# Kernel optimization log

Hardware: AMD Instinct MI355X
Metric: run time of the kernel (lower is better)

Reference implementation:

```python
import jax, jax.numpy as jnp
import numpy as np


def setup_inputs() -> dict:
    key = jax.random.key(0)
    ks = jax.random.split(key, 8)
    B = 65536
    x = jax.random.normal(ks[0], (B, 784), dtype=jnp.float32)
    conv_w = jnp.ones((3, 3), dtype=jnp.float32)  # Parameter(ones((3,3)))
    # Linear layers stored as (in, out) weight + (out,) bias
    def lin(k, fin, fout):
        kw, kb = jax.random.split(k)
        bound = 1.0 / np.sqrt(fin)
        W = jax.random.uniform(kw, (fin, fout), minval=-bound, maxval=bound, dtype=jnp.float32)
        b = jax.random.uniform(kb, (fout,), minval=-bound, maxval=bound, dtype=jnp.float32)
        return W, b
    W1, b1 = lin(ks[1], 26 * 26, 500)
    W2, b2 = lin(ks[2], 500, 200)
    W3, b3 = lin(ks[3], 200, 10)
    return {"x": x, "conv_w": conv_w, "W1": W1, "b1": b1,
            "W2": W2, "b2": b2, "W3": W3, "b3": b3}


def reference(x, conv_w, W1, b1, W2, b2, W3, b3):
    B = x.shape[0]
    img = x.reshape(B, 1, 28, 28)  # NCHW, single channel
    kern = conv_w.reshape(1, 1, 3, 3)  # OIHW
    # valid 2D cross-correlation == torch tensordot sliding-window loop
    conv = jax.lax.conv_general_dilated(
        img, kern, window_strides=(1, 1), padding='VALID',
        dimension_numbers=('NCHW', 'OIHW', 'NCHW'))  # (B,1,26,26)
    h = conv.reshape(B, 26 * 26)
    h = jax.nn.relu(h @ W1 + b1)
    h = jax.nn.relu(h @ W2 + b2)
    return h @ W3 + b3  # (B, 10) logits
```

## Files before the change

kernel.cpp:

```cpp
#include <hip/hip_runtime.h>
#include <hip/hip_bf16.h>
#include <stdint.h>

typedef __bf16 bf16x8 __attribute__((ext_vector_type(8)));
typedef float  f32x4  __attribute__((ext_vector_type(4)));


#define KT1 25
#define NF1 32
#define KT2 16
#define NF2 16
#define KT3 8

__global__ void prep_w1(const float* __restrict__ W1, const float* __restrict__ cw,
                        __bf16* __restrict__ w1s) {
  int gid  = blockIdx.x * 256 + threadIdx.x;
  int lane = gid & 63;
  int slot = gid >> 6;
  int t = slot >> 5;
  int f = slot & 31;
  int kbase = t * 32 + ((lane >> 4) << 3);
  int n = f * 16 + (lane & 15);
  float c[9];
#pragma unroll
  for (int i = 0; i < 9; ++i) c[i] = cw[i];
  bf16x8 v;
#pragma unroll
  for (int e = 0; e < 8; ++e) {
    int k = kbase + e;
    float acc = 0.f;
    if (k < 784 && n < 500) {
      int pi = k / 28, pj = k % 28;
#pragma unroll
      for (int dr = 0; dr < 3; ++dr) {
        int r = pi - dr;
        if (r < 0 || r >= 26) continue;
#pragma unroll
        for (int dc = 0; dc < 3; ++dc) {
          int cc = pj - dc;
          if (cc < 0 || cc >= 26) continue;
          acc += c[dr * 3 + dc] * W1[(size_t)(r * 26 + cc) * 500 + n];
        }
      }
    }
    v[e] = (__bf16)acc;
  }
  *(bf16x8*)(w1s + (size_t)(slot * 64 + lane) * 8) = v;
}

__global__ void prep_w2(const float* __restrict__ W2, __bf16* __restrict__ w2s) {
  int gid  = blockIdx.x * 256 + threadIdx.x;
  int lane = gid & 63;
  int slot = gid >> 6;
  int t = slot >> 4;
  int f = slot & 15;
  int kbase = t * 32 + ((lane >> 4) << 3);
  int n = f * 16 + (lane & 15);
  bf16x8 v;
#pragma unroll
  for (int e = 0; e < 8; ++e) {
    int k = kbase + e;
    float val = (k < 500 && n < 200) ? W2[(size_t)k * 200 + n] : 0.f;
    v[e] = (__bf16)val;
  }
  *(bf16x8*)(w2s + (size_t)(slot * 64 + lane) * 8) = v;
}

__global__ void prep_w3(const float* __restrict__ W3, __bf16* __restrict__ w3s) {
  int gid  = blockIdx.x * 256 + threadIdx.x;
  int lane = gid & 63;
  int t    = gid >> 6;
  int kbase = t * 32 + ((lane >> 4) << 3);
  int n = lane & 15;
  bf16x8 v;
#pragma unroll
  for (int e = 0; e < 8; ++e) {
    int k = kbase + e;
    float val = (k < 200 && n < 10) ? W3[(size_t)k * 10 + n] : 0.f;
    v[e] = (__bf16)val;
  }
  *(bf16x8*)(w3s + (size_t)(t * 64 + lane) * 8) = v;
}

__global__ __launch_bounds__(256, 2) void mlp_fused(
    const float* __restrict__ x,
    const __bf16* __restrict__ w1s, const __bf16* __restrict__ w2s,
    const __bf16* __restrict__ w3s,
    const float* __restrict__ b1, const float* __restrict__ b2,
    const float* __restrict__ b3,
    float* __restrict__ out)
{
  __shared__ __align__(16) char smem[64 * 1024];
  __shared__ float sb1[512];
  __shared__ float sb2[256];

  const int tid  = threadIdx.x;
  const int lane = tid & 63;
  const int w    = tid >> 6;
  const int lrow = lane & 15;
  const int lgrp = lane >> 4;
  const int brow = blockIdx.x * 64;
  const int xr   = tid >> 2;
  const int xq   = tid & 3;

  sb1[tid]       = (tid < 500) ? b1[tid] : 0.f;
  sb1[tid + 256] = (tid + 256 < 500) ? b1[tid + 256] : 0.f;
  sb2[tid]       = (tid < 200) ? b2[tid] : 0.f;

  const f32x4 FZ = {0.f, 0.f, 0.f, 0.f};

  f32x4 acc1[4][8];
#pragma unroll
  for (int m = 0; m < 4; ++m)
#pragma unroll
    for (int f = 0; f < 8; ++f) acc1[m][f] = FZ;

  const bf16x8* w1p   = (const bf16x8*)w1s + ((size_t)(w * 8) * 64 + lane);
  const float*  xbase = x + (size_t)(brow + xr) * 784;
  const int     xoff  = xr * 64 + ((xq ^ (xr & 3)) << 4);

  f32x4 g[4][2];

  auto gload4 = [&](int s) {
#pragma unroll
    for (int j = 0; j < 4; ++j) {
      int tile = s * 4 + j;
      if (tile > 24) tile = 24;
      int gk = tile * 32 + xq * 8;
      if (gk > 776) gk = 776;
      const float* p = xbase + gk;
      g[j][0] = *(const f32x4*)p;
      g[j][1] = *(const f32x4*)(p + 4);
    }
  };
  auto cwrite4 = [&](int buf) {
#pragma unroll
    for (int j = 0; j < 4; ++j) {
      bf16x8 v;
#pragma unroll
      for (int e = 0; e < 4; ++e) { v[e] = (__bf16)g[j][0][e]; v[e + 4] = (__bf16)g[j][1][e]; }
      *(bf16x8*)(smem + buf * 16384 + j * 4096 + xoff) = v;
    }
  };

  bf16x8 bA[8], bB[8];

  auto ktile = [&](int tile, int rb, int slot, bf16x8 (&bc)[8], bf16x8 (&bn)[8], bool pf) {
    bf16x8 afr[4];
#pragma unroll
    for (int m = 0; m < 4; ++m) {
      int r = m * 16 + lrow;
      afr[m] = *(const bf16x8*)(smem + rb + slot * 4096 + r * 64 + ((lgrp ^ (r & 3)) << 4));
    }
    if (pf) {
#pragma unroll
      for (int f = 0; f < 8; ++f) bn[f] = w1p[(size_t)((tile + 1) * NF1 + f) * 64];
    }
    __builtin_amdgcn_s_setprio(1);
#pragma unroll
    for (int f = 0; f < 8; ++f)
#pragma unroll
      for (int m = 0; m < 4; ++m)
        acc1[m][f] = __builtin_amdgcn_mfma_f32_16x16x32_bf16(afr[m], bc[f], acc1[m][f], 0, 0, 0);
    __builtin_amdgcn_s_setprio(0);
  };

  gload4(0);
#pragma unroll
  for (int f = 0; f < 8; ++f) bA[f] = w1p[(size_t)f * 64];
  cwrite4(0);
  asm volatile("s_waitcnt lgkmcnt(0)\n\ts_barrier" ::: "memory");

  for (int s = 0; s < 6; ++s) {
    int rb = (s & 1) * 16384;
    gload4(s + 1);
    int t0 = s * 4;
    ktile(t0 + 0, rb, 0, bA, bB, true);
    ktile(t0 + 1, rb, 1, bB, bA, true);
    ktile(t0 + 2, rb, 2, bA, bB, true);
    ktile(t0 + 3, rb, 3, bB, bA, true);
    cwrite4((s + 1) & 1);
    asm volatile("s_waitcnt lgkmcnt(0)\n\ts_barrier" ::: "memory");
  }
  ktile(24, 0, 0, bA, bB, false);

  const bf16x8* w2p = (const bf16x8*)w2s + ((size_t)(w * 4) * 64 + lane);
  bf16x8 b2a[4], b2b[4];
#pragma unroll
  for (int f = 0; f < 4; ++f) b2a[f] = w2p[(size_t)f * 64];

  asm volatile("s_waitcnt lgkmcnt(0)\n\ts_barrier" ::: "memory");

#pragma unroll
  for (int m = 0; m < 4; ++m) {
#pragma unroll
    for (int f = 0; f < 8; ++f) {
      int col = w * 128 + f * 16 + lrow;
      float bias = sb1[col];
#pragma unroll
      for (int r = 0; r < 4; ++r) {
        int row = m * 16 + lgrp * 4 + r;
        float v = fmaxf(acc1[m][f][r] + bias, 0.f);
        int off = row * 1024 + ((col * 2) ^ ((row & 7) << 4));
        *(__bf16*)(smem + off) = (__bf16)v;
      }
    }
  }
  __syncthreads();

  f32x4 acc2[4][4];
#pragma unroll
  for (int m = 0; m < 4; ++m)
#pragma unroll
    for (int f = 0; f < 4; ++f) acc2[m][f] = FZ;

  for (int t = 0; t < KT2; t += 2) {
#pragma unroll
    for (int f = 0; f < 4; ++f) b2b[f] = w2p[(size_t)((t + 1) * NF2 + f) * 64];
    {
      bf16x8 a2[4];
#pragma unroll
      for (int m = 0; m < 4; ++m) {
        int row = m * 16 + lrow;
        int off = row * 1024 + ((t * 64 + lgrp * 16) ^ ((row & 7) << 4));
        a2[m] = *(const bf16x8*)(smem + off);
      }
      __builtin_amdgcn_s_setprio(1);
#pragma unroll
      for (int f = 0; f < 4; ++f)
#pragma unroll
        for (int m = 0; m < 4; ++m)
          acc2[m][f] = __builtin_amdgcn_mfma_f32_16x16x32_bf16(a2[m], b2a[f], acc2[m][f], 0, 0, 0);
      __builtin_amdgcn_s_setprio(0);
    }
#pragma unroll
    for (int f = 0; f < 4; ++f) b2a[f] = w2p[(size_t)((t + 2) * NF2 + f) * 64];
    {
      bf16x8 a2[4];
#pragma unroll
      for (int m = 0; m < 4; ++m) {
        int row = m * 16 + lrow;
        int off = row * 1024 + (((t + 1) * 64 + lgrp * 16) ^ ((row & 7) << 4));
        a2[m] = *(const bf16x8*)(smem + off);
      }
      __builtin_amdgcn_s_setprio(1);
#pragma unroll
      for (int f = 0; f < 4; ++f)
#pragma unroll
        for (int m = 0; m < 4; ++m)
          acc2[m][f] = __builtin_amdgcn_mfma_f32_16x16x32_bf16(a2[m], b2b[f], acc2[m][f], 0, 0, 0);
      __builtin_amdgcn_s_setprio(0);
    }
  }

  __syncthreads();

#pragma unroll
  for (int m = 0; m < 4; ++m) {
#pragma unroll
    for (int f = 0; f < 4; ++f) {
      int col = w * 64 + f * 16 + lrow;
      float bias = sb2[col];
#pragma unroll
      for (int r = 0; r < 4; ++r) {
        int row = m * 16 + lgrp * 4 + r;
        float v = fmaxf(acc2[m][f][r] + bias, 0.f);
        int off = row * 512 + ((col * 2) ^ ((row & 7) << 4));
        *(__bf16*)(smem + off) = (__bf16)v;
      }
    }
  }
  __syncthreads();

  {
    f32x4 a3 = FZ;
    const bf16x8* w3p = (const bf16x8*)w3s + lane;
#pragma unroll
    for (int t = 0; t < KT3; ++t) {
      int row = w * 16 + lrow;
      int off = row * 512 + ((t * 64 + lgrp * 16) ^ ((row & 7) << 4));
      bf16x8 a = *(const bf16x8*)(smem + off);
      a3 = __builtin_amdgcn_mfma_f32_16x16x32_bf16(a, w3p[(size_t)t * 64], a3, 0, 0, 0);
    }
    if (lrow < 10) {
      float bias = b3[lrow];
#pragma unroll
      for (int r = 0; r < 4; ++r)
        out[(size_t)(brow + w * 16 + lgrp * 4 + r) * 10 + lrow] = a3[r] + bias;
    }
  }
}

extern "C" void kernel_launch(void* const* d_in, const int* in_sizes, int n_in,
                              void* d_out, int out_size, void* d_ws, size_t ws_size,
                              hipStream_t stream) {
  const float* x  = (const float*)d_in[0];
  const float* cw = (const float*)d_in[1];
  const float* W1 = (const float*)d_in[2];
  const float* b1 = (const float*)d_in[3];
  const float* W2 = (const float*)d_in[4];
  const float* b2 = (const float*)d_in[5];
  const float* W3 = (const float*)d_in[6];
  const float* b3 = (const float*)d_in[7];
  float* out = (float*)d_out;

  __bf16* w1s = (__bf16*)d_ws;
  __bf16* w2s = w1s + (size_t)KT1 * NF1 * 64 * 8;
  __bf16* w3s = w2s + (size_t)KT2 * NF2 * 64 * 8;

  prep_w1<<<200, 256, 0, stream>>>(W1, cw, w1s);
  prep_w2<<<64, 256, 0, stream>>>(W2, w2s);
  prep_w3<<<2, 256, 0, stream>>>(W3, w3s);

  mlp_fused<<<65536 / 64, 256, 0, stream>>>(x, w1s, w2s, w3s, b1, b2, b3, out);
}
```

Measured before the change: 99.66 us.

## Use 128-row blocks of 512 threads with W1 tiles staged through LDS

Doubles the block tile to 128 rows with eight waves in a 2x4 grid, so each W1 tile is loaded once per block into LDS via global_load_lds and shared by both row groups, instead of each wave reading B fragments from global memory. The x staging switches from four-tile chunks to per-tile double buffering, with a vmcnt wait overlapping loads of tile t+1 with compute on tile t. LDS grows to 128KB and occupancy drops to one block per CU, which adds a barrier every k-tile and gives less latency hiding. The layer-3 section was not updated for 128 rows in the visible portion, so correctness depends on the hidden code.

```diff
diff --git a/kernel.cpp b/kernel.cpp
--- a/kernel.cpp
+++ b/kernel.cpp
@@ -82,7 +82,12 @@
   *(bf16x8*)(w3s + (size_t)(t * 64 + lane) * 8) = v;
 }
 
-__global__ __launch_bounds__(256, 2) void mlp_fused(
+#define BS0 0
+#define BS1 32768
+#define XS0 65536
+#define XS1 73728
+
+__global__ __launch_bounds__(512, 1) void mlp_fused(
     const float* __restrict__ x,
     const __bf16* __restrict__ w1s, const __bf16* __restrict__ w2s,
     const __bf16* __restrict__ w3s,
@@ -90,22 +95,23 @@
     const float* __restrict__ b3,
     float* __restrict__ out)
 {
-  __shared__ __align__(16) char smem[64 * 1024];
+  __shared__ __align__(16) char smem[128 * 1024];
   __shared__ float sb1[512];
   __shared__ float sb2[256];
 
   const int tid  = threadIdx.x;
   const int lane = tid & 63;
   const int w    = tid >> 6;
+  const int mg   = w >> 2;
+  const int ng   = w & 3;
   const int lrow = lane & 15;
   const int lgrp = lane >> 4;
-  const int brow = blockIdx.x * 64;
+  const int brow = blockIdx.x * 128;
   const int xr   = tid >> 2;
   const int xq   = tid & 3;
 
-  sb1[tid]       = (tid < 500) ? b1[tid] : 0.f;
-  sb1[tid + 256] = (tid + 256 < 500) ? b1[tid + 256] : 0.f;
-  sb2[tid]       = (tid < 200) ? b2[tid] : 0.f;
+  sb1[tid & 511] = ((tid & 511) < 500) ? b1[tid & 511] : 0.f;
+  if (tid < 256) sb2[tid] = (tid < 200) ? b2[tid] : 0.f;
 
   const f32x4 FZ = {0.f, 0.f, 0.f, 0.f};
 
@@ -115,91 +121,87 @@
 #pragma unroll
     for (int f = 0; f < 8; ++f) acc1[m][f] = FZ;
 
-  const bf16x8* w1p   = (const bf16x8*)w1s + ((size_t)(w * 8) * 64 + lane);
-  const float*  xbase = x + (size_t)(brow + xr) * 784;
-  const int     xoff  = xr * 64 + ((xq ^ (xr & 3)) << 4);
-
-  f32x4 g[4][2];
-
-  auto gload4 = [&](int s) {
-#pragma unroll
-    for (int j = 0; j < 4; ++j) {
-      int tile = s * 4 + j;
-      if (tile > 24) tile = 24;
-      int gk = tile * 32 + xq * 8;
-      if (gk > 776) gk = 776;
-      const float* p = xbase + gk;
-      g[j][0] = *(const f32x4*)p;
-      g[j][1] = *(const f32x4*)(p + 4);
-    }
-  };
-  auto cwrite4 = [&](int buf) {
-#pragma unroll
-    for (int j = 0; j < 4; ++j) {
-      bf16x8 v;
-#pragma unroll
-      for (int e = 0; e < 4; ++e) { v[e] = (__bf16)g[j][0][e]; v[e + 4] = (__bf16)g[j][1][e]; }
-      *(bf16x8*)(smem + buf * 16384 + j * 4096 + xoff) = v;
-    }
-  };
-
-  bf16x8 bA[8], bB[8];
-
-  auto ktile = [&](int tile, int rb, int slot, bf16x8 (&bc)[8], bf16x8 (&bn)[8], bool pf) {
-    bf16x8 afr[4];
+  const float* xbase = x + (size_t)(brow + xr) * 784;
+  const int    xwoff = xr * 64 + ((xq ^ (xr & 3)) << 4);
+
+  f32x4 g[2];
+
+  auto xload = [&](int t) {
+    int gk = t * 32 + xq * 8;
+    if (gk > 776) gk = 776;
+    g[0] = *(const f32x4*)(xbase + gk);
+    g[1] = *(const f32x4*)(xbase + gk + 4);
+  };
+  auto xwrite = [&](int buf) {
+    bf16x8 v;
+#pragma unroll
+    for (int e = 0; e < 4; ++e) { v[e] = (__bf16)g[0][e]; v[e + 4] = (__bf16)g[1][e]; }
+    *(bf16x8*)(smem + buf + xwoff) = v;
+  };
+  auto stage_b = [&](int tile, int buf) {
+    const char* src = (const char*)w1s + (size_t)tile * 32768 + w * 4096 + lane * 16;
+#pragma unroll
+    for (int i = 0; i < 4; ++i)
+      __builtin_amdgcn_global_load_lds(
+          (const __attribute__((address_space(1))) void*)(src + i * 1024),
+          (__attribute__((address_space(3))) void*)(smem + buf + w * 4096 + i * 1024),
+          16, 0, 0);
+  };
+  auto ktile = [&](int xbuf, int bbuf) {
+    bf16x8 afr[4], bfr[8];
 #pragma unroll
     for (int m = 0; m < 4; ++m) {
-      int r = m * 16 + lrow;
-      afr[m] = *(const bf16x8*)(smem + rb + slot * 4096 + r * 64 + ((lgrp ^ (r & 3)) << 4));
-    }
-    if (pf) {
-#pragma unroll
-      for (int f = 0; f < 8; ++f) bn[f] = w1p[(size_t)((tile + 1) * NF1 + f) * 64];
-    }
+      int r = mg * 64 + m * 16 + lrow;
+      afr[m] = *(const bf16x8*)(smem + xbuf + r * 64 + ((lgrp ^ (r & 3)) << 4));
+    }
+#pragma unroll
+    for (int f = 0; f < 8; ++f)
+      bfr[f] = *(const bf16x8*)(smem + bbuf + (ng * 8 + f) * 1024 + lane * 16);
     __builtin_amdgcn_s_setprio(1);
 #pragma unroll
     for (int f = 0; f < 8; ++f)
 #pragma unroll
       for (int m = 0; m < 4; ++m)
-        acc1[m][f] = __builtin_amdgcn_mfma_f32_16x16x32_bf16(afr[m], bc[f], acc1[m][f], 0, 0, 0);
+        acc1[m][f] = __builtin_amdgcn_mfma_f32_16x16x32_bf16(afr[m], bfr[f], acc1[m][f], 0, 0, 0);
     __builtin_amdgcn_s_setprio(0);
   };
-
-  gload4(0);
-#pragma unroll
-  for (int f = 0; f < 8; ++f) bA[f] = w1p[(size_t)f * 64];
-  cwrite4(0);
-  asm volatile("s_waitcnt lgkmcnt(0)\n\ts_barrier" ::: "memory");
-
-  for (int s = 0; s < 6; ++s) {
-    int rb = (s & 1) * 16384;
-    gload4(s + 1);
-    int t0 = s * 4;
-    ktile(t0 + 0, rb, 0, bA, bB, true);
-    ktile(t0 + 1, rb, 1, bB, bA, true);
-    ktile(t0 + 2, rb, 2, bA, bB, true);
-    ktile(t0 + 3, rb, 3, bB, bA, true);
-    cwrite4((s + 1) & 1);
+  auto body = [&](int t, int xcur, int bcur, int xnxt, int bnxt) {
+    xload(t + 1);
+    stage_b(t + 1, bnxt);
+    asm volatile("s_waitcnt vmcnt(6)" ::: "memory");
+    ktile(xcur, bcur);
+    xwrite(xnxt);
     asm volatile("s_waitcnt lgkmcnt(0)\n\ts_barrier" ::: "memory");
-  }
-  ktile(24, 0, 0, bA, bB, false);
-
-  const bf16x8* w2p = (const bf16x8*)w2s + ((size_t)(w * 4) * 64 + lane);
+  };
+
+  xload(0);
+  stage_b(0, BS0);
+  xwrite(0 + XS0);
+  asm volatile("s_waitcnt vmcnt(0) lgkmcnt(0)\n\ts_barrier" ::: "memory");
+
+  for (int t = 0; t < 24; t += 2) {
+    body(t,     XS0, BS0, XS1, BS1);
+    body(t + 1, XS1, BS1, XS0, BS0);
+  }
+  asm volatile("s_waitcnt vmcnt(0)" ::: "memory");
+  ktile(XS0, BS0);
+
+  const bf16x8* w2p = (const bf16x8*)w2s + ((size_t)(ng * 4) * 64 + lane);
   bf16x8 b2a[4], b2b[4];
 #pragma unroll
   for (int f = 0; f < 4; ++f) b2a[f] = w2p[(size_t)f * 64];
 
-  asm volatile("s_waitcnt lgkmcnt(0)\n\ts_barrier" ::: "memory");
+  __syncthreads();
 
 #pragma unroll
   for (int m = 0; m < 4; ++m) {
 #pragma unroll
     for (int f = 0; f < 8; ++f) {
-      int col = w * 128 + f * 16 + lrow;
+      int col = ng * 128 + f * 16 + lrow;
       float bias = sb1[col];
 #pragma unroll
       for (int r = 0; r < 4; ++r) {
-        int row = m * 16 + lgrp * 4 + r;
+        int row = mg * 64 + m * 16 + lgrp * 4 + r;
         float v = fmaxf(acc1[m][f][r] + bias, 0.f);
         int off = row * 1024 + ((col * 2) ^ ((row & 7) << 4));
         *(__bf16*)(smem + off) = (__bf16)v;
@@ -221,7 +223,7 @@
       bf16x8 a2[4];
 #pragma unroll
       for (int m = 0; m < 4; ++m) {
-        int row = m * 16 + lrow;
+        int row = mg * 64 + m * 16 + lrow;
         int off = row * 1024 + ((t * 64 + lgrp * 16) ^ ((row & 7) << 4));
         a2[m] = *(const bf16x8*)(smem + off);
       }
@@ -239,7 +241,7 @@
       bf16x8 a2[4];
 #pragma unroll
       for (int m = 0; m < 4; ++m) {
-        int row = m * 16 + lrow;
+        int row = mg * 64 + m * 16 + lrow;
         int off = row * 1024 + (((t + 1) * 64 + lgrp * 16) ^ ((row & 7) << 4));
         a2[m] = *(const bf16x8*)(smem + off);
       }
@@ -259,11 +261,11 @@
   for (int m = 0; m < 4; ++m) {
 #pragma unroll
     for (int f = 0; f < 4; ++f) {
-      int col = w * 64 + f * 16 + lrow;
+      int col = ng * 64 + f * 16 + lrow;
       float bias = sb2[col];
 #pragma unroll
       for (int r = 0; r < 4; ++r) {
-        int row = m * 16 + lgrp * 4 + r;
+        int row = mg * 64 + m * 16 + lgrp * 4 + r;
         float v = fmaxf(acc2[m][f][r] + bias, 0.f);
         int off = row * 512 + ((col * 2) ^ ((row & 7) << 4));
         *(__bf16*)(smem + off) = (__bf16)v;
@@ -312,5 +314,5 @@
   prep_w2<<<64, 256, 0, stream>>>(W2, w2s);
   prep_w3<<<2, 256, 0, stream>>>(W3, w3s);
 
-  mlp_fused<<<65536 / 64, 256, 0, stream>>>(x, w1s, w2s, w3s, b1, b2, b3, out);
-}
+  mlp_fused<<<65536 / 128, 512, 0, stream>>>(x, w1s, w2s, w3s, b1, b2, b3, out);
+}
```

Result: slower. 108.1 us, median of 2 (+8.5%).
